# Optimization experiments

Hardware: AMD Instinct MI355X
Metric: run time of the kernel (lower is better)

The kernel has to match this reference:

```python
import jax, jax.numpy as jnp
import numpy as np

LAMBDA_N = 0.01
OUTER_LOOP = 2
INNER_LOOP = 50
MAX_DIST = 0.1
LR = 0.2
LR_DECAY = 0.1
ADAGRAD_EPS = 1e-10


def _normalize(x, eps=1e-12):
    # torch F.normalize: x / max(||x||, eps)
    n = jnp.linalg.norm(x, axis=-1, keepdims=True)
    return x / jnp.maximum(n, eps)


def _interp_bary(tri, vw):
    # tri: [b, n, 3, 3] (3 corners x 3 coords), vw: [b, n, 2]
    bary = jnp.concatenate([vw, 1.0 - vw[..., :1] - vw[..., 1:2]], axis=-1)  # [b,n,3]
    return jnp.einsum('bnij,bni->bnj', tri, bary)


def setup_inputs() -> dict:
    key = jax.random.key(0)
    k0, k1, k2, k3, k4 = jax.random.split(key, 5)
    B, Np, Nv, Nf = 1, 8192, 16384, 16384
    query_V = jax.random.uniform(k0, (B, Np, 3), dtype=jnp.float32)
    query_N = _normalize(jax.random.normal(k1, (B, Np, 3), dtype=jnp.float32))
    mesh_V = jax.random.uniform(k2, (Nv, 3), dtype=jnp.float32)
    mesh_F = jax.random.randint(k3, (Nf, 3), 0, Nv, dtype=jnp.int64)
    mesh_N = _normalize(jax.random.normal(k4, (Nv, 3), dtype=jnp.float32))
    return {'query_V': query_V, 'query_N': query_N, 'mesh_V': mesh_V,
            'mesh_F': mesh_F, 'mesh_N': mesh_N}


def reference(query_V, query_N, mesh_V, mesh_F, mesh_N):
    # ---- init_corres_spt: brute-force KNN (K=1) to face centers ----
    F_centers = mesh_V[mesh_F].mean(axis=1)                     # [Nf, 3]
    # squared distances [B, Np, Nf] (pytorch3d knn_points returns squared dist)
    d2 = (jnp.sum(query_V * query_V, axis=-1, keepdims=True)
          - 2.0 * jnp.einsum('bnd,fd->bnf', query_V, F_centers)
          + jnp.sum(F_centers * F_centers, axis=-1))
    spt_fidx = jnp.argmin(d2, axis=-1)                          # [B, Np]
    dmin = jnp.min(d2, axis=-1)
    outlier_mask = dmin > MAX_DIST
    valid = ~outlier_mask
    mask = valid.astype(query_V.dtype)                          # [B, Np]
    denom = jnp.maximum(jnp.sum(mask), 1.0)

    spt_vw0 = jnp.full(query_V.shape[:-1] + (2,), 1.0 / 3.0, dtype=query_V.dtype)

    tri = mesh_F[spt_fidx]          # [B, Np, 3] vertex indices (gather)
    tri_V = mesh_V[tri]             # [B, Np, 3, 3]
    tri_N = mesh_N[tri]             # [B, Np, 3, 3]

    def loss_fn(delta, vw_base):
        vw = vw_base + delta
        corres_V = _interp_bary(tri_V, vw)
        loss_v = jnp.linalg.norm(corres_V - query_V, axis=-1)   # [B, Np]
        corres_N = _normalize(_interp_bary(tri_N, vw))
        loss_n = jnp.linalg.norm(corres_N - query_N, axis=-1)
        per_point = loss_v + LAMBDA_N * loss_n
        # masked mean over valid points only (original indexes out valid points)
        return jnp.sum(per_point * mask) / denom

    grad_fn = jax.grad(loss_fn)

    def solve_delta_vw(vw_base):
        # Adagrad(lr=0.2, lr_decay=0.1), 50 steps
        def step(carry, i):
            delta, ssum = carry
            g = grad_fn(delta, vw_base)
            ssum = ssum + g * g
            clr = LR / (1.0 + i * LR_DECAY)
            delta = delta - clr * g / (jnp.sqrt(ssum) + ADAGRAD_EPS)
            return (delta, ssum), None
        z = jnp.zeros_like(vw_base)
        (delta, _), _ = jax.lax.scan(step, (z, z),
                                     jnp.arange(INNER_LOOP, dtype=vw_base.dtype))
        return delta

    # ---- update_corres_spt: outer loop with alpha halving ----
    vw = spt_vw0
    alpha = 1.0
    for _ in range(OUTER_LOOP):
        delta = solve_delta_vw(vw)
        vw = vw + delta * alpha       # triwalk fallback: spt_vw + spt_delta
        alpha = alpha * 0.5

    # invalid (outlier) points keep their init barycentric coords
    spt_vw = jnp.where(valid[..., None], vw, spt_vw0)
    return spt_fidx, spt_vw, outlier_mask
```

## Files before the change

### kernel.cpp

```cpp
#include <hip/hip_runtime.h>
#include <math.h>

#define NP 8192
#define NF 16384
#define GQ 8
#define SPLIT 2
#define NFS (NF / SPLIT)
#define NG (NP / GQ)

__global__ __launch_bounds__(256) void k_centers(const float* __restrict__ mV,
                                                 const int* __restrict__ mF,
                                                 double* __restrict__ ctr,
                                                 double* __restrict__ clrtab) {
    if (blockIdx.x == 0 && threadIdx.x < 50) {
        clrtab[threadIdx.x] = 0.2 / (1.0 + (double)threadIdx.x * 0.1);
    }
    int f = blockIdx.x * 256 + threadIdx.x;
    if (f >= NF) return;
    int i0 = mF[3*f+0], i1 = mF[3*f+1], i2 = mF[3*f+2];
    double cx = ((double)mV[3*i0+0] + (double)mV[3*i1+0] + (double)mV[3*i2+0]) / 3.0;
    double cy = ((double)mV[3*i0+1] + (double)mV[3*i1+1] + (double)mV[3*i2+1]) / 3.0;
    double cz = ((double)mV[3*i0+2] + (double)mV[3*i1+2] + (double)mV[3*i2+2]) / 3.0;
    ctr[4*f+0] = cx; ctr[4*f+1] = cy; ctr[4*f+2] = cz;
    ctr[4*f+3] = cx*cx + cy*cy + cz*cz;
}

__global__ __launch_bounds__(256) void k_knn_part(const float* __restrict__ qV,
                                                  const double* __restrict__ ctr,
                                                  double* __restrict__ pkey,
                                                  int* __restrict__ pidx) {
    int g = blockIdx.x / SPLIT;
    int s = blockIdx.x % SPLIT;
    int pbase = g * GQ;
    int fbase = s * NFS;

    double qx[GQ], qy[GQ], qz[GQ];
    #pragma unroll
    for (int gg = 0; gg < GQ; ++gg) {
        int p = pbase + gg;
        qx[gg] = (double)qV[3*p+0];
        qy[gg] = (double)qV[3*p+1];
        qz[gg] = (double)qV[3*p+2];
    }
    double best[GQ]; int bidx[GQ];
    #pragma unroll
    for (int gg = 0; gg < GQ; ++gg) { best[gg] = 1e300; bidx[gg] = 0x7fffffff; }

    const double4* ctr4 = (const double4*)ctr;
    #pragma unroll 2
    for (int fo = threadIdx.x; fo < NFS; fo += 256) {
        int f = fbase + fo;
        double4 c = ctr4[f];
        #pragma unroll
        for (int gg = 0; gg < GQ; ++gg) {
            double dot = qx[gg]*c.x + qy[gg]*c.y + qz[gg]*c.z;
            double key = c.w - 2.0*dot;
            if (key < best[gg]) { best[gg] = key; bidx[gg] = f; }
        }
    }
    #pragma unroll
    for (int off = 32; off > 0; off >>= 1) {
        #pragma unroll
        for (int gg = 0; gg < GQ; ++gg) {
            double ov = __shfl_down(best[gg], off);
            int    oi = __shfl_down(bidx[gg], off);
            if (ov < best[gg] || (ov == best[gg] && oi < bidx[gg])) { best[gg] = ov; bidx[gg] = oi; }
        }
    }
    __shared__ double sv[4][GQ];
    __shared__ int    si[4][GQ];
    int wid = threadIdx.x >> 6, lane = threadIdx.x & 63;
    if (lane == 0) {
        #pragma unroll
        for (int gg = 0; gg < GQ; ++gg) { sv[wid][gg] = best[gg]; si[wid][gg] = bidx[gg]; }
    }
    __syncthreads();
    if (threadIdx.x == 0) {
        for (int gg = 0; gg < GQ; ++gg) {
            double bv = sv[0][gg]; int bi = si[0][gg];
            for (int w2 = 1; w2 < 4; ++w2) {
                double ov = sv[w2][gg]; int oi = si[w2][gg];
                if (ov < bv || (ov == bv && oi < bi)) { bv = ov; bi = oi; }
            }
            int slot = (g * SPLIT + s) * GQ + gg;
            pkey[slot] = bv;
            pidx[slot] = bi;
        }
    }
}

__global__ __launch_bounds__(256) void k_finish(const float* __restrict__ qV,
                                                const double* __restrict__ ctr,
                                                const double* __restrict__ pkey,
                                                const int* __restrict__ pidx,
                                                float* __restrict__ out,
                                                int* __restrict__ fidx_ws,
                                                int* __restrict__ valid_ws) {
    int p = blockIdx.x * 256 + threadIdx.x;
    if (p >= NP) return;
    int g = p / GQ, j = p % GQ;
    double bv = 1e300; int bi = 0x7fffffff;
    #pragma unroll
    for (int s = 0; s < SPLIT; ++s) {
        int slot = (g * SPLIT + s) * GQ + j;
        double ov = pkey[slot]; int oi = pidx[slot];
        if (ov < bv || (ov == bv && oi < bi)) { bv = ov; bi = oi; }
    }
    const double4* ctr4 = (const double4*)ctr;
    double4 c = ctr4[bi];
    double qx = (double)qV[3*p+0], qy = (double)qV[3*p+1], qz = (double)qV[3*p+2];
    double dot = qx*c.x + qy*c.y + qz*c.z;
    double qq  = qx*qx + qy*qy + qz*qz;
    double d2  = (qq - 2.0*dot) + c.w;
    int outlier = (d2 > 0.1) ? 1 : 0;
    fidx_ws[p]  = bi;
    valid_ws[p] = 1 - outlier;
    out[p]        = (float)bi;
    out[3*NP + p] = outlier ? 1.0f : 0.0f;
}

__global__ __launch_bounds__(256) void k_denom(const int* __restrict__ valid_ws,
                                               double* __restrict__ denom) {
    __shared__ int s[256];
    int acc = 0;
    for (int i = threadIdx.x; i < NP; i += 256) acc += valid_ws[i];
    s[threadIdx.x] = acc;
    __syncthreads();
    for (int off = 128; off > 0; off >>= 1) {
        if (threadIdx.x < off) s[threadIdx.x] += s[threadIdx.x + off];
        __syncthreads();
    }
    if (threadIdx.x == 0) {
        double d = (double)s[0];
        denom[0] = d > 1.0 ? d : 1.0;
    }
}

__global__ __launch_bounds__(256) void k_opt(const float* __restrict__ qV,
                                             const float* __restrict__ qN,
                                             const float* __restrict__ mV,
                                             const int* __restrict__ mF,
                                             const float* __restrict__ mN,
                                             const int* __restrict__ fidx_ws,
                                             const int* __restrict__ valid_ws,
                                             const double* __restrict__ denomp,
                                             const double* __restrict__ clrtab,
                                             float* __restrict__ out) {
    int p = blockIdx.x * 256 + threadIdx.x;
    if (p >= NP) return;
    const float third = (float)(1.0/3.0);
    if (!valid_ws[p]) {
        out[NP + 2*p + 0] = third;
        out[NP + 2*p + 1] = third;
        return;
    }
    double inv_denom = 1.0 / denomp[0];
    int f = fidx_ws[p];
    int i0 = mF[3*f+0], i1 = mF[3*f+1], i2 = mF[3*f+2];

    double V0x = mV[3*i0+0], V0y = mV[3*i0+1], V0z = mV[3*i0+2];
    double V1x = mV[3*i1+0], V1y = mV[3*i1+1], V1z = mV[3*i1+2];
    double V2x = mV[3*i2+0], V2y = mV[3*i2+1], V2z = mV[3*i2+2];
    double N0x = mN[3*i0+0], N0y = mN[3*i0+1], N0z = mN[3*i0+2];
    double N1x = mN[3*i1+0], N1y = mN[3*i1+1], N1z = mN[3*i1+2];
    double N2x = mN[3*i2+0], N2y = mN[3*i2+1], N2z = mN[3*i2+2];
    double qx  = qV[3*p+0],  qy  = qV[3*p+1],  qz  = qV[3*p+2];
    double qnx = qN[3*p+0],  qny = qN[3*p+1],  qnz = qN[3*p+2];

    double Eux = V0x - V2x, Euy = V0y - V2y, Euz = V0z - V2z;
    double Ewx = V1x - V2x, Ewy = V1y - V2y, Ewz = V1z - V2z;
    double Fux = N0x - N2x, Fuy = N0y - N2y, Fuz = N0z - N2z;
    double Fwx = N1x - N2x, Fwy = N1y - N2y, Fwz = N1z - N2z;
    double Kx  = V2x - qx,  Ky  = V2y - qy,  Kz  = V2z - qz;

    double u = 1.0/3.0, w = 1.0/3.0;
    double alpha = 1.0;
    for (int outer = 0; outer < 2; ++outer) {
        double du = 0.0, dw = 0.0, su = 0.0, sw = 0.0;
        for (int it = 0; it < 50; ++it) {
            double uu = u + du, ww = w + dw;
            double rvx = uu*Eux + ww*Ewx + Kx;
            double rvy = uu*Euy + ww*Ewy + Ky;
            double rvz = uu*Euz + ww*Ewz + Kz;
            double L2v = rvx*rvx + rvy*rvy + rvz*rvz;
            double invLv = rsqrt(L2v);
            double gu = (rvx*Eux + rvy*Euy + rvz*Euz) * invLv;
            double gw = (rvx*Ewx + rvy*Ewy + rvz*Ewz) * invLv;
            double nx = uu*Fux + ww*Fwx + N2x;
            double ny = uu*Fuy + ww*Fwy + N2y;
            double nz = uu*Fuz + ww*Fwz + N2z;
            double m2 = nx*nx + ny*ny + nz*nz;
            bool   mok = (m2 > 1e-24);
            double inv = mok ? rsqrt(m2) : 1e12;
            double hx = nx*inv, hy = ny*inv, hz = nz*inv;
            double rnx = hx - qnx, rny = hy - qny, rnz = hz - qnz;
            double L2n = rnx*rnx + rny*rny + rnz*rnz;
            double invLn = rsqrt(L2n);
            double A_u = rnx*Fux + rny*Fuy + rnz*Fuz;
            double A_w = rnx*Fwx + rny*Fwy + rnz*Fwz;
            double B   = rnx*nx + rny*ny + rnz*nz;
            double C_u = nx*Fux + ny*Fuy + nz*Fuz;
            double C_w = nx*Fwx + ny*Fwy + nz*Fwz;
            double s = mok ? ((B*inv)*inv)*inv : 0.0;
            double gnu = (A_u*inv - s*C_u) * invLn;
            double gnw = (A_w*inv - s*C_w) * invLn;
            gu = (gu + 0.01*gnu) * inv_denom;
            gw = (gw + 0.01*gnw) * inv_denom;
            su += gu*gu; sw += gw*gw;
            double clr = clrtab[it];
            du -= clr * gu / (sqrt(su) + 1e-10);
            dw -= clr * gw / (sqrt(sw) + 1e-10);
        }
        u += du * alpha; w += dw * alpha;
        alpha *= 0.5;
    }
    out[NP + 2*p + 0] = (float)u;
    out[NP + 2*p + 1] = (float)w;
}

extern "C" void kernel_launch(void* const* d_in, const int* in_sizes, int n_in,
                              void* d_out, int out_size, void* d_ws, size_t ws_size,
                              hipStream_t stream) {
    const float* qV = (const float*)d_in[0];
    const float* qN = (const float*)d_in[1];
    const float* mV = (const float*)d_in[2];
    const int*   mF = (const int*)d_in[3];
    const float* mN = (const float*)d_in[4];
    float* out = (float*)d_out;

    double* ctr      = (double*)d_ws;
    double* denom    = ctr + (size_t)NF*4;
    double* clrtab   = denom + 1;
    double* pkey     = clrtab + 50;
    int*    pidx     = (int*)(pkey + (size_t)NP*SPLIT);
    int*    fidx_ws  = pidx + (size_t)NP*SPLIT;
    int*    valid_ws = fidx_ws + NP;

    hipLaunchKernelGGL(k_centers,  dim3(NF/256),   dim3(256), 0, stream, mV, mF, ctr, clrtab);
    hipLaunchKernelGGL(k_knn_part, dim3(NG*SPLIT), dim3(256), 0, stream, qV, ctr, pkey, pidx);
    hipLaunchKernelGGL(k_finish,   dim3(NP/256),   dim3(256), 0, stream, qV, ctr, pkey, pidx,
                       out, fidx_ws, valid_ws);
    hipLaunchKernelGGL(k_denom,    dim3(1),        dim3(256), 0, stream, valid_ws, denom);
    hipLaunchKernelGGL(k_opt,      dim3(NP/256),   dim3(256), 0, stream,
                       qV, qN, mV, mF, mN, fidx_ws, valid_ws, denom, clrtab, out);
}
```

Baseline: 104.8 us.

## Map one query per thread in KNN, scanning face slices with broadcast loads

Result: slower. 152.9 us (+45.8%).

```diff
diff --git a/kernel.cpp b/kernel.cpp
--- a/kernel.cpp
+++ b/kernel.cpp
@@ -3,10 +3,10 @@
 
 #define NP 8192
 #define NF 16384
-#define GQ 8
-#define SPLIT 2
+#define SPLIT 16
 #define NFS (NF / SPLIT)
-#define NG (NP / GQ)
+#define PB  256
+#define NPB (NP / PB)
 
 __global__ __launch_bounds__(256) void k_centers(const float* __restrict__ mV,
                                                  const int* __restrict__ mF,
@@ -31,62 +31,25 @@
                                                   int* __restrict__ pidx) {
     int g = blockIdx.x / SPLIT;
     int s = blockIdx.x % SPLIT;
-    int pbase = g * GQ;
+    int p = g * PB + threadIdx.x;
+
+    double qx = (double)qV[3*p+0];
+    double qy = (double)qV[3*p+1];
+    double qz = (double)qV[3*p+2];
+    double best = 1e300; int bi = 0x7fffffff;
+
+    const double4* ctr4 = (const double4*)ctr;
     int fbase = s * NFS;
-
-    double qx[GQ], qy[GQ], qz[GQ];
-    #pragma unroll
-    for (int gg = 0; gg < GQ; ++gg) {
-        int p = pbase + gg;
-        qx[gg] = (double)qV[3*p+0];
-        qy[gg] = (double)qV[3*p+1];
-        qz[gg] = (double)qV[3*p+2];
-    }
-    double best[GQ]; int bidx[GQ];
-    #pragma unroll
-    for (int gg = 0; gg < GQ; ++gg) { best[gg] = 1e300; bidx[gg] = 0x7fffffff; }
-
-    const double4* ctr4 = (const double4*)ctr;
-    #pragma unroll 2
-    for (int fo = threadIdx.x; fo < NFS; fo += 256) {
-        int f = fbase + fo;
+    #pragma unroll 4
+    for (int i = 0; i < NFS; ++i) {
+        int f = fbase + i;
         double4 c = ctr4[f];
-        #pragma unroll
-        for (int gg = 0; gg < GQ; ++gg) {
-            double dot = qx[gg]*c.x + qy[gg]*c.y + qz[gg]*c.z;
-            double key = c.w - 2.0*dot;
-            if (key < best[gg]) { best[gg] = key; bidx[gg] = f; }
-        }
-    }
-    #pragma unroll
-    for (int off = 32; off > 0; off >>= 1) {
-        #pragma unroll
-        for (int gg = 0; gg < GQ; ++gg) {
-            double ov = __shfl_down(best[gg], off);
-            int    oi = __shfl_down(bidx[gg], off);
-            if (ov < best[gg] || (ov == best[gg] && oi < bidx[gg])) { best[gg] = ov; bidx[gg] = oi; }
-        }
-    }
-    __shared__ double sv[4][GQ];
-    __shared__ int    si[4][GQ];
-    int wid = threadIdx.x >> 6, lane = threadIdx.x & 63;
-    if (lane == 0) {
-        #pragma unroll
-        for (int gg = 0; gg < GQ; ++gg) { sv[wid][gg] = best[gg]; si[wid][gg] = bidx[gg]; }
-    }
-    __syncthreads();
-    if (threadIdx.x == 0) {
-        for (int gg = 0; gg < GQ; ++gg) {
-            double bv = sv[0][gg]; int bi = si[0][gg];
-            for (int w2 = 1; w2 < 4; ++w2) {
-                double ov = sv[w2][gg]; int oi = si[w2][gg];
-                if (ov < bv || (ov == bv && oi < bi)) { bv = ov; bi = oi; }
-            }
-            int slot = (g * SPLIT + s) * GQ + gg;
-            pkey[slot] = bv;
-            pidx[slot] = bi;
-        }
-    }
+        double dot = qx*c.x + qy*c.y + qz*c.z;
+        double key = c.w - 2.0*dot;
+        if (key < best) { best = key; bi = f; }
+    }
+    pkey[(size_t)s*NP + p] = best;
+    pidx[(size_t)s*NP + p] = bi;
 }
 
 __global__ __launch_bounds__(256) void k_finish(const float* __restrict__ qV,
@@ -98,12 +61,11 @@
                                                 int* __restrict__ valid_ws) {
     int p = blockIdx.x * 256 + threadIdx.x;
     if (p >= NP) return;
-    int g = p / GQ, j = p % GQ;
     double bv = 1e300; int bi = 0x7fffffff;
     #pragma unroll
     for (int s = 0; s < SPLIT; ++s) {
-        int slot = (g * SPLIT + s) * GQ + j;
-        double ov = pkey[slot]; int oi = pidx[slot];
+        double ov = pkey[(size_t)s*NP + p];
+        int    oi = pidx[(size_t)s*NP + p];
         if (ov < bv || (ov == bv && oi < bi)) { bv = ov; bi = oi; }
     }
     const double4* ctr4 = (const double4*)ctr;
@@ -232,15 +194,15 @@
     double* denom    = ctr + (size_t)NF*4;
     double* clrtab   = denom + 1;
     double* pkey     = clrtab + 50;
-    int*    pidx     = (int*)(pkey + (size_t)NP*SPLIT);
-    int*    fidx_ws  = pidx + (size_t)NP*SPLIT;
+    int*    pidx     = (int*)(pkey + (size_t)SPLIT*NP);
+    int*    fidx_ws  = pidx + (size_t)SPLIT*NP;
     int*    valid_ws = fidx_ws + NP;
 
-    hipLaunchKernelGGL(k_centers,  dim3(NF/256),   dim3(256), 0, stream, mV, mF, ctr, clrtab);
-    hipLaunchKernelGGL(k_knn_part, dim3(NG*SPLIT), dim3(256), 0, stream, qV, ctr, pkey, pidx);
-    hipLaunchKernelGGL(k_finish,   dim3(NP/256),   dim3(256), 0, stream, qV, ctr, pkey, pidx,
+    hipLaunchKernelGGL(k_centers,  dim3(NF/256),    dim3(256), 0, stream, mV, mF, ctr, clrtab);
+    hipLaunchKernelGGL(k_knn_part, dim3(NPB*SPLIT), dim3(256), 0, stream, qV, ctr, pkey, pidx);
+    hipLaunchKernelGGL(k_finish,   dim3(NP/256),    dim3(256), 0, stream, qV, ctr, pkey, pidx,
                        out, fidx_ws, valid_ws);
-    hipLaunchKernelGGL(k_denom,    dim3(1),        dim3(256), 0, stream, valid_ws, denom);
-    hipLaunchKernelGGL(k_opt,      dim3(NP/256),   dim3(256), 0, stream,
+    hipLaunchKernelGGL(k_denom,    dim3(1),         dim3(256), 0, stream, valid_ws, denom);
+    hipLaunchKernelGGL(k_opt,      dim3(NP/256),    dim3(256), 0, stream,
                        qV, qN, mV, mF, mN, fidx_ws, valid_ws, denom, clrtab, out);
 }
```
